# Kernel tuning notes

Measured on AMD Instinct MI355X. Metric: run time of the kernel, lower is better.

## Reference

```python
import jax, jax.numpy as jnp
import numpy as np

HEADS = 8

def group_conv1x1(x, w, heads):
    # x: (B, Cin, H, W); w: (Cout, Cin//heads, 1, 1) grouped 1x1 conv, no bias
    B, Cin, H, W = x.shape
    Cout = w.shape[0]
    xg = x.reshape(B, heads, Cin // heads, H * W)
    wg = w[:, :, 0, 0].reshape(heads, Cout // heads, Cin // heads)
    out = jnp.einsum('hoc,bhcl->bhol', wg, xg)
    return out.reshape(B, Cout, H, W)

def sine_pe(d_model, length):
    # standard transformer sin/cos encoding, laid out as (d_model, length)
    pos = jnp.arange(length, dtype=jnp.float32)
    i = jnp.arange(0, d_model, 2, dtype=jnp.float32)
    div = jnp.exp(-(jnp.log(10000.0)) * i / d_model)
    ang = div[:, None] * pos[None, :]            # (d/2, L)
    pe = jnp.zeros((d_model, length), dtype=jnp.float32)
    pe = pe.at[0::2].set(jnp.sin(ang)).at[1::2].set(jnp.cos(ang))
    return pe

def setup_inputs() -> dict:
    key = jax.random.key(0)
    k0, k1, k2, k3 = jax.random.split(key, 4)
    B, Cin, H, W = 16, 256, 32, 32
    Cout, heads = 256, HEADS
    fan_out = Cout  # kaiming_normal fan_out for 1x1 conv = Cout*1*1
    std = np.sqrt(2.0 / fan_out)
    x = jax.random.normal(k0, (B, Cin, H, W), dtype=jnp.float32)
    wq = jax.random.normal(k1, (Cout, Cin // heads, 1, 1), dtype=jnp.float32) * std
    wk = jax.random.normal(k2, (Cout, Cin // heads, 1, 1), dtype=jnp.float32) * std
    wv = jax.random.normal(k3, (Cout, Cin // heads, 1, 1), dtype=jnp.float32) * std
    return {"x": x, "wq": wq, "wk": wk, "wv": wv}

def reference(x, wq, wk, wv):
    B, Cin, H, W = x.shape
    Cout = wq.shape[0]
    heads = HEADS
    dh = Cout // heads
    L = H * W

    q = group_conv1x1(x, wq, heads)              # (B, Cout, H, W)
    k = group_conv1x1(x, wk, heads)
    v = group_conv1x1(x, wv, heads)

    # sine positional encoding added to keys over flattened spatial positions
    k = k.reshape(B, Cout, L) + sine_pe(Cout, L)[None]

    q = q.reshape(B, heads, dh, L)               # (B, h, dh, L)
    k = k.reshape(B, heads, dh, L)
    v = v.reshape(B, heads, dh, L)

    scores = jnp.einsum('bhdq,bhdk->bhqk', q, k)  # (B, h, L, L) -- no sqrt(d) scaling, as in source
    attn = jax.nn.softmax(scores, axis=-1)
    out = jnp.einsum('bhqk,bhdk->bhdq', attn, v)  # (B, h, dh, L)
    return out.reshape(B, Cout, H, W)
```

## Files before the change

kernel.cpp:

```cpp
#include <hip/hip_runtime.h>

#define LL   1024
#define BHD  128
#define LOG2E 1.44269504088896340736f

typedef unsigned int       uint;
typedef unsigned short     ushort;
typedef unsigned long long ull;

typedef __attribute__((ext_vector_type(8)))  __bf16          bf16x8;
typedef __attribute__((ext_vector_type(8)))  unsigned short  u16x8;
typedef __attribute__((ext_vector_type(4)))  unsigned short  u16x4;
typedef __attribute__((ext_vector_type(4)))  uint            ui32x4;
typedef __attribute__((ext_vector_type(4)))  float           f32x4;
typedef __attribute__((ext_vector_type(16))) float           f32x16;

static __device__ __forceinline__ ushort f2bf(float f){
  union {float f; uint u;} v; v.f = f;
  uint u = v.u + 0x7fffu + ((v.u >> 16) & 1u);
  return (ushort)(u >> 16);
}
static __device__ __forceinline__ uint pack2(float a, float b){
  return (uint)f2bf(a) | ((uint)f2bf(b) << 16);
}
static __device__ __forceinline__ uint packtrunc(float a, float b){
  union {float f; uint u;} x, y; x.f = a; y.f = b;
  return __builtin_amdgcn_perm(y.u, x.u, 0x07060302u);
}
static __device__ __forceinline__ bf16x8 ld_frag(const ushort* p){
  u16x8 t = *(const u16x8*)p;
  return __builtin_bit_cast(bf16x8, t);
}
static __device__ __forceinline__ bf16x8 ld_frag64(const ushort* p){
  u16x4 a = *(const u16x4*)p;
  u16x4 b = *(const u16x4*)(p + 4);
  u16x8 t;
  t[0]=a[0]; t[1]=a[1]; t[2]=a[2]; t[3]=a[3];
  t[4]=b[0]; t[5]=b[1]; t[6]=b[2]; t[7]=b[3];
  return __builtin_bit_cast(bf16x8, t);
}

static __device__ __forceinline__ bool sniff_is_bf16(const uint* xw, int tid, int* cnt){
  uint w = xw[tid & 255];
  uint e = (w >> 7) & 0xFFu;
  bool hit = (e >= 118u) && (e <= 132u);
  ull b = __ballot(hit);
  if ((tid & 63) == 0) cnt[tid >> 6] = __popcll(b);
  __syncthreads();
  bool r = (cnt[0] + cnt[1] + cnt[2] + cnt[3]) > 128;
  __syncthreads();
  return r;
}

__global__ __launch_bounds__(256) void qkv_kernel(
    const void* __restrict__ xr,
    const void* __restrict__ wqr,
    const void* __restrict__ wkr,
    const void* __restrict__ wvr,
    ushort* __restrict__ Qt, ushort* __restrict__ Kt, ushort* __restrict__ Vt)
{
  const int bh   = blockIdx.x;
  const int lt   = blockIdx.y;
  const int tid  = threadIdx.x;
  const int wave = tid >> 6;
  const int lane = tid & 63;
  const int l16  = lane & 15;
  const int quad = lane >> 4;
  const int lbase = lt * 128;

  __shared__ int cnt[4];
  __shared__ __align__(16) uint xsd[128][20];

  const bool is_bf = sniff_is_bf16((const uint*)xr, tid, cnt);

  {
    const int cp = tid & 15, lg = tid >> 4;
    const size_t rb = (size_t)(bh*32 + 2*cp)*LL + lbase + lg*8;
    uint dw[8];
    if (is_bf){
      u16x8 e = *(const u16x8*)((const ushort*)xr + rb);
      u16x8 o = *(const u16x8*)((const ushort*)xr + rb + LL);
      #pragma unroll
      for (int j = 0; j < 8; ++j) dw[j] = (uint)e[j] | ((uint)o[j] << 16);
    } else {
      const float* xf = (const float*)xr;
      float4 e0 = *(const float4*)(xf + rb);
      float4 e1 = *(const float4*)(xf + rb + 4);
      float4 o0 = *(const float4*)(xf + rb + LL);
      float4 o1 = *(const float4*)(xf + rb + LL + 4);
      dw[0]=pack2(e0.x,o0.x); dw[1]=pack2(e0.y,o0.y);
      dw[2]=pack2(e0.z,o0.z); dw[3]=pack2(e0.w,o0.w);
      dw[4]=pack2(e1.x,o1.x); dw[5]=pack2(e1.y,o1.y);
      dw[6]=pack2(e1.z,o1.z); dw[7]=pack2(e1.w,o1.w);
    }
    #pragma unroll
    for (int j = 0; j < 8; ++j) xsd[lg*8 + j][cp] = dw[j];
  }
  __syncthreads();

  const void* wsrc[3] = {wqr, wkr, wvr};
  bf16x8 bw[3][2];
  #pragma unroll
  for (int p = 0; p < 3; ++p)
    #pragma unroll
    for (int nh = 0; nh < 2; ++nh){
      const int row = (bh & 7)*32 + nh*16 + l16;
      if (is_bf){
        bw[p][nh] = ld_frag((const ushort*)wsrc[p] + (size_t)row*32 + quad*8);
      } else {
        const float* wf = (const float*)wsrc[p] + (size_t)row*32 + quad*8;
        float4 f0 = *(const float4*)wf, f1 = *(const float4*)(wf + 4);
        u16x8 t;
        t[0]=f2bf(f0.x); t[1]=f2bf(f0.y); t[2]=f2bf(f0.z); t[3]=f2bf(f0.w);
        t[4]=f2bf(f1.x); t[5]=f2bf(f1.y); t[6]=f2bf(f1.z); t[7]=f2bf(f1.w);
        bw[p][nh] = __builtin_bit_cast(bf16x8, t);
      }
    }

  bf16x8 ax[2];
  #pragma unroll
  for (int mt = 0; mt < 2; ++mt)
    ax[mt] = __builtin_bit_cast(bf16x8,
               *(const ui32x4*)&xsd[wave*32 + mt*16 + l16][quad*4]);

  const f32x4 z = {0.f,0.f,0.f,0.f};
  f32x4 dq[2][2], dk[2][2], dv[2][2];
  #pragma unroll
  for (int mt = 0; mt < 2; ++mt)
    #pragma unroll
    for (int nh = 0; nh < 2; ++nh){
      dq[mt][nh] = __builtin_amdgcn_mfma_f32_16x16x32_bf16(ax[mt], bw[0][nh], z, 0,0,0);
      dk[mt][nh] = __builtin_amdgcn_mfma_f32_16x16x32_bf16(ax[mt], bw[1][nh], z, 0,0,0);
      dv[nh][mt] = __builtin_amdgcn_mfma_f32_16x16x32_bf16(bw[2][nh], ax[mt], z, 0,0,0);
    }

  #pragma unroll
  for (int mt = 0; mt < 2; ++mt)
    #pragma unroll
    for (int nh = 0; nh < 2; ++nh)
      #pragma unroll
      for (int r = 0; r < 4; ++r){
        const int l = lbase + wave*32 + mt*16 + quad*4 + r;
        const int d = nh*16 + l16;
        Qt[((size_t)bh*LL + l)*32 + d] = f2bf(dq[mt][nh][r]);
      }
  #pragma unroll
  for (int mt = 0; mt < 2; ++mt)
    #pragma unroll
    for (int nh = 0; nh < 2; ++nh){
      const int d = nh*16 + l16;
      const int c = (bh & 7)*32 + d;
      const float freq = __expf(-0.03597789207f * (float)(c & ~1));
      #pragma unroll
      for (int r = 0; r < 4; ++r){
        const int l = lbase + wave*32 + mt*16 + quad*4 + r;
        const float ang = freq * (float)l;
        const float pe  = (c & 1) ? __cosf(ang) : __sinf(ang);
        Kt[((size_t)bh*LL + l)*32 + d] = f2bf((dk[mt][nh][r] + pe) * LOG2E);
      }
    }
  #pragma unroll
  for (int dh = 0; dh < 2; ++dh)
    #pragma unroll
    for (int mt = 0; mt < 2; ++mt)
      #pragma unroll
      for (int r = 0; r < 4; ++r){
        const int d = dh*16 + quad*4 + r;
        const int l = lbase + wave*32 + mt*16 + l16;
        Vt[((size_t)(bh*32 + d))*LL + l] = f2bf(dv[dh][mt][r]);
      }
}

__global__ __launch_bounds__(256, 4) void attn_kernel(
    const void*   __restrict__ xr,
    const ushort* __restrict__ Qt,
    const ushort* __restrict__ Kt,
    const ushort* __restrict__ Vt,
    void* __restrict__ out)
{
  const int bh  = blockIdx.x;
  const int qt  = blockIdx.y;
  const int tid = threadIdx.x;
  const int wave = tid >> 6;
  const int lane = tid & 63;
  const int q32  = lane & 31;
  const int h    = lane >> 5;

  __shared__ int cnt[4];
  __shared__ __align__(16) ushort Ks[64][40];
  __shared__ __align__(16) ushort Vs[32][68];

  const bool is_bf = sniff_is_bf16((const uint*)xr, tid, cnt);

  const int qg = qt*128 + wave*32 + q32;
  const ushort* qrow = Qt + ((size_t)bh*LL + qg)*32;
  bf16x8 bq0 = ld_frag(qrow + h*8);
  bf16x8 bq1 = ld_frag(qrow + 16 + h*8);

  const int skey = tid >> 2, sseg = tid & 3;
  const int sp = (sseg + (skey >> 2)) & 3;
  const ushort* kg = Kt + ((size_t)(bh*LL + skey))*32 + sseg*8;
  ushort* kw = &Ks[skey][sp*8];
  const int sd = tid >> 3, sg = tid & 7;
  const ushort* vg = Vt + ((size_t)(bh*32 + sd))*LL + sg*8;
  ushort* vw = &Vs[sd][sg*8];

  const int rot = (q32 >> 2) & 3;
  const ushort* ka0 = &Ks[q32][((h + rot) & 3)*8];
  const ushort* ka1 = &Ks[q32][((2 + h + rot) & 3)*8];
  const ushort* vr  = &Vs[q32][h*8];

  f32x16 O = {};
  float rsum = 0.f;

  u16x8 kreg = *(const u16x8*)kg;
  u16x8 vreg = *(const u16x8*)vg;

  for (int kt = 0; kt < 16; ++kt){
    __syncthreads();
    *(u16x8*)kw = kreg;
    { u16x4 lo, hi;
      lo[0]=vreg[0]; lo[1]=vreg[1]; lo[2]=vreg[2]; lo[3]=vreg[3];
      hi[0]=vreg[4]; hi[1]=vreg[5]; hi[2]=vreg[6]; hi[3]=vreg[7];
      *(u16x4*)vw = lo; *(u16x4*)(vw + 4) = hi; }
    __syncthreads();
    if (kt < 15){
      kreg = *(const u16x8*)(kg + (size_t)(kt+1)*64*32);
      vreg = *(const u16x8*)(vg + (kt+1)*64);
    }

    f32x16 st[2];
    #pragma unroll
    for (int t = 0; t < 2; ++t){
      bf16x8 a0 = ld_frag(ka0 + t*32*40);
      bf16x8 a1 = ld_frag(ka1 + t*32*40);
      f32x16 zz = {};
      f32x16 s  = __builtin_amdgcn_mfma_f32_32x32x16_bf16(a0, bq0, zz, 0,0,0);
      st[t]     = __builtin_amdgcn_mfma_f32_32x32x16_bf16(a1, bq1, s,  0,0,0);
    }

    uint pr[2][8];
    #pragma unroll
    for (int t = 0; t < 2; ++t)
      #pragma unroll
      for (int zi = 0; zi < 8; ++zi){
        float p0 = __builtin_amdgcn_exp2f(st[t][2*zi]);
        float p1 = __builtin_amdgcn_exp2f(st[t][2*zi+1]);
        rsum += p0 + p1;
        pr[t][zi] = packtrunc(p0, p1);
      }

    #pragma unroll
    for (int c = 0; c < 4; ++c){
      const int t = c >> 1, g0 = 4*(c & 1);
      uint s0 = h ? pr[t][g0+0] : pr[t][g0+2];
      uint s1 = h ? pr[t][g0+1] : pr[t][g0+3];
      uint r0 = (uint)__shfl_xor((int)s0, 32);
      uint r1 = (uint)__shfl_xor((int)s1, 32);
      ui32x4 pb;
      pb[0] = h ? r0 : pr[t][g0+0];
      pb[1] = h ? r1 : pr[t][g0+1];
      pb[2] = h ? pr[t][g0+2] : r0;
      pb[3] = h ? pr[t][g0+3] : r1;
      bf16x8 va = ld_frag64(vr + c*16);
      O = __builtin_amdgcn_mfma_f32_32x32x16_bf16(
            va, __builtin_bit_cast(bf16x8, pb), O, 0,0,0);
    }
  }

  rsum += __shfl_xor(rsum, 32);
  const float inv = 1.f / rsum;

  #pragma unroll
  for (int reg = 0; reg < 16; ++reg){
    const int d = (reg & 3) + 8*(reg >> 2) + 4*h;
    const float v = O[reg] * inv;
    const size_t off = ((size_t)(bh*32 + d))*LL + qg;
    if (is_bf) ((ushort*)out)[off] = f2bf(v);
    else       ((float*)out)[off]  = v;
  }
}

extern "C" void kernel_launch(void* const* d_in, const int* in_sizes, int n_in,
                              void* d_out, int out_size, void* d_ws, size_t ws_size,
                              hipStream_t stream) {
  const void* x  = d_in[0];
  const void* wq = d_in[1];
  const void* wk = d_in[2];
  const void* wv = d_in[3];

  ushort* Qt = (ushort*)d_ws;
  ushort* Kt = Qt + (size_t)BHD * LL * 32;
  ushort* Vt = Kt + (size_t)BHD * LL * 32;

  qkv_kernel <<<dim3(BHD, 8), 256, 0, stream>>>(x, wq, wk, wv, Qt, Kt, Vt);
  attn_kernel<<<dim3(BHD, 8), 256, 0, stream>>>(x, Qt, Kt, Vt, d_out);
}
```

Baseline: 113.1 us.

## Double key tile to 128 and compute softmax row sums via MFMA with ones

Key/value tiles per iteration grow from 64 to 128 keys, halving the number of barrier-separated loop iterations and the global load rounds. The per-element scalar accumulation of exp values is replaced with an extra MFMA that multiplies the packed probabilities by a ones matrix. That MFMA yields row sums consistent with the truncated bf16 values actually used, and it frees VALU work. The cost is doubled MFMA count in the PV stage and larger shared memory per block, which may reduce occupancy.

New measurement: 114.2 us. No clear change (+1.0%).

```diff
diff --git a/kernel.cpp b/kernel.cpp
--- a/kernel.cpp
+++ b/kernel.cpp
@@ -187,8 +187,8 @@
   const int h    = lane >> 5;
 
   __shared__ int cnt[4];
-  __shared__ __align__(16) ushort Ks[64][40];
-  __shared__ __align__(16) ushort Vs[32][68];
+  __shared__ __align__(16) ushort Ks[128][40];
+  __shared__ __align__(16) ushort Vs[32][132];
 
   const bool is_bf = sniff_is_bf16((const uint*)xr, tid, cnt);
 
@@ -197,13 +197,20 @@
   bf16x8 bq0 = ld_frag(qrow + h*8);
   bf16x8 bq1 = ld_frag(qrow + 16 + h*8);
 
-  const int skey = tid >> 2, sseg = tid & 3;
-  const int sp = (sseg + (skey >> 2)) & 3;
-  const ushort* kg = Kt + ((size_t)(bh*LL + skey))*32 + sseg*8;
-  ushort* kw = &Ks[skey][sp*8];
+  bf16x8 ones;
+  { u16x8 t;
+    #pragma unroll
+    for (int j = 0; j < 8; ++j) t[j] = 0x3F80u;
+    ones = __builtin_bit_cast(bf16x8, t); }
+
+  const int skey = tid >> 1, shalf = tid & 1;
+  const int rotw = (skey >> 2) & 3;
+  const ushort* kg0 = Kt + ((size_t)(bh*LL + skey))*32 + (2*shalf)*8;
+  ushort* kw0 = &Ks[skey][((2*shalf     + rotw) & 3)*8];
+  ushort* kw1 = &Ks[skey][((2*shalf + 1 + rotw) & 3)*8];
   const int sd = tid >> 3, sg = tid & 7;
-  const ushort* vg = Vt + ((size_t)(bh*32 + sd))*LL + sg*8;
-  ushort* vw = &Vs[sd][sg*8];
+  const ushort* vgp = Vt + ((size_t)(bh*32 + sd))*LL + sg*16;
+  ushort* vw = &Vs[sd][sg*16];
 
   const int rot = (q32 >> 2) & 3;
   const ushort* ka0 = &Ks[q32][((h + rot) & 3)*8];
@@ -211,65 +218,79 @@
   const ushort* vr  = &Vs[q32][h*8];
 
   f32x16 O = {};
-  float rsum = 0.f;
-
-  u16x8 kreg = *(const u16x8*)kg;
-  u16x8 vreg = *(const u16x8*)vg;
-
-  for (int kt = 0; kt < 16; ++kt){
+  f32x16 R = {};
+
+  u16x8 k0 = *(const u16x8*)kg0;
+  u16x8 k1 = *(const u16x8*)(kg0 + 8);
+  u16x8 v0 = *(const u16x8*)vgp;
+  u16x8 v1 = *(const u16x8*)(vgp + 8);
+
+  for (int it = 0; it < 8; ++it){
     __syncthreads();
-    *(u16x8*)kw = kreg;
-    { u16x4 lo, hi;
-      lo[0]=vreg[0]; lo[1]=vreg[1]; lo[2]=vreg[2]; lo[3]=vreg[3];
-      hi[0]=vreg[4]; hi[1]=vreg[5]; hi[2]=vreg[6]; hi[3]=vreg[7];
-      *(u16x4*)vw = lo; *(u16x4*)(vw + 4) = hi; }
+    *(ui32x4*)kw0 = __builtin_bit_cast(ui32x4, k0);
+    *(ui32x4*)kw1 = __builtin_bit_cast(ui32x4, k1);
+    {
+      u16x4 a, b;
+      a[0]=v0[0]; a[1]=v0[1]; a[2]=v0[2]; a[3]=v0[3];
+      b[0]=v0[4]; b[1]=v0[5]; b[2]=v0[6]; b[3]=v0[7];
+      *(u16x4*)vw = a; *(u16x4*)(vw + 4) = b;
+      a[0]=v1[0]; a[1]=v1[1]; a[2]=v1[2]; a[3]=v1[3];
+      b[0]=v1[4]; b[1]=v1[5]; b[2]=v1[6]; b[3]=v1[7];
+      *(u16x4*)(vw + 8) = a; *(u16x4*)(vw + 12) = b;
+    }
     __syncthreads();
-    if (kt < 15){
-      kreg = *(const u16x8*)(kg + (size_t)(kt+1)*64*32);
-      vreg = *(const u16x8*)(vg + (kt+1)*64);
-    }
-
-    f32x16 st[2];
-    #pragma unroll
-    for (int t = 0; t < 2; ++t){
-      bf16x8 a0 = ld_frag(ka0 + t*32*40);
-      bf16x8 a1 = ld_frag(ka1 + t*32*40);
-      f32x16 zz = {};
-      f32x16 s  = __builtin_amdgcn_mfma_f32_32x32x16_bf16(a0, bq0, zz, 0,0,0);
-      st[t]     = __builtin_amdgcn_mfma_f32_32x32x16_bf16(a1, bq1, s,  0,0,0);
-    }
-
-    uint pr[2][8];
-    #pragma unroll
-    for (int t = 0; t < 2; ++t)
-      #pragma unroll
-      for (int zi = 0; zi < 8; ++zi){
-        float p0 = __builtin_amdgcn_exp2f(st[t][2*zi]);
-        float p1 = __builtin_amdgcn_exp2f(st[t][2*zi+1]);
-        rsum += p0 + p1;
-        pr[t][zi] = packtrunc(p0, p1);
-      }
-
-    #pragma unroll
-    for (int c = 0; c < 4; ++c){
-      const int t = c >> 1, g0 = 4*(c & 1);
-      uint s0 = h ? pr[t][g0+0] : pr[t][g0+2];
-      uint s1 = h ? pr[t][g0+1] : pr[t][g0+3];
-      uint r0 = (uint)__shfl_xor((int)s0, 32);
-      uint r1 = (uint)__shfl_xor((int)s1, 32);
-      ui32x4 pb;
-      pb[0] = h ? r0 : pr[t][g0+0];
-      pb[1] = h ? r1 : pr[t][g0+1];
-      pb[2] = h ? pr[t][g0+2] : r0;
-      pb[3] = h ? pr[t][g0+3] : r1;
-      bf16x8 va = ld_frag64(vr + c*16);
-      O = __builtin_amdgcn_mfma_f32_32x32x16_bf16(
-            va, __builtin_bit_cast(bf16x8, pb), O, 0,0,0);
+    if (it < 7){
+      const int ko = (it + 1)*128;
+      k0 = *(const u16x8*)(kg0 + (size_t)ko*32);
+      k1 = *(const u16x8*)(kg0 + (size_t)ko*32 + 8);
+      v0 = *(const u16x8*)(vgp + ko);
+      v1 = *(const u16x8*)(vgp + ko + 8);
+    }
+
+    #pragma unroll
+    for (int u = 0; u < 2; ++u){
+      f32x16 st[2];
+      #pragma unroll
+      for (int tt = 0; tt < 2; ++tt){
+        const int t = 2*u + tt;
+        bf16x8 a0 = ld_frag(ka0 + t*32*40);
+        bf16x8 a1 = ld_frag(ka1 + t*32*40);
+        f32x16 zz = {};
+        f32x16 s  = __builtin_amdgcn_mfma_f32_32x32x16_bf16(a0, bq0, zz, 0,0,0);
+        st[tt]    = __builtin_amdgcn_mfma_f32_32x32x16_bf16(a1, bq1, s,  0,0,0);
+      }
+
+      uint pr[2][8];
+      #pragma unroll
+      for (int tt = 0; tt < 2; ++tt)
+        #pragma unroll
+        for (int zi = 0; zi < 8; ++zi){
+          float p0 = __builtin_amdgcn_exp2f(st[tt][2*zi]);
+          float p1 = __builtin_amdgcn_exp2f(st[tt][2*zi+1]);
+          pr[tt][zi] = packtrunc(p0, p1);
+        }
+
+      #pragma unroll
+      for (int c = 0; c < 4; ++c){
+        const int tt = c >> 1, g0 = 4*(c & 1);
+        uint s0 = h ? pr[tt][g0+0] : pr[tt][g0+2];
+        uint s1 = h ? pr[tt][g0+1] : pr[tt][g0+3];
+        uint r0 = (uint)__shfl_xor((int)s0, 32);
+        uint r1 = (uint)__shfl_xor((int)s1, 32);
+        ui32x4 pb;
+        pb[0] = h ? r0 : pr[tt][g0+0];
+        pb[1] = h ? r1 : pr[tt][g0+1];
+        pb[2] = h ? pr[tt][g0+2] : r0;
+        pb[3] = h ? pr[tt][g0+3] : r1;
+        bf16x8 pf = __builtin_bit_cast(bf16x8, pb);
+        bf16x8 va = ld_frag64(vr + (u*4 + c)*16);
+        O = __builtin_amdgcn_mfma_f32_32x32x16_bf16(va,   pf, O, 0,0,0);
+        R = __builtin_amdgcn_mfma_f32_32x32x16_bf16(ones, pf, R, 0,0,0);
+      }
     }
   }
 
-  rsum += __shfl_xor(rsum, 32);
-  const float inv = 1.f / rsum;
+  const float inv = 1.f / R[0];
 
   #pragma unroll
   for (int reg = 0; reg < 16; ++reg){
```
